# Optimization experiments

Measured on AMD Instinct MI355X. Metric: run time of the kernel, lower is better.

The kernel has to match this reference:

```python
import jax, jax.numpy as jnp
import numpy as np


def expm2(M):
    """Closed-form exponential of a batch of 2x2 matrices M[..., 2, 2].

    exp(M) = e^m * (f*I + g*(M - m*I)) with m = tr(M)/2,
    delta = m^2 - det(M), and (f, g) = (cosh s, sinh s / s) if delta >= 0
    else (cos s, sin s / s) with s = sqrt(|delta|). Identical math to
    torch.matrix_exp for 2x2 inputs.
    """
    a, b, c, d = M[..., 0, 0], M[..., 0, 1], M[..., 1, 0], M[..., 1, 1]
    m = 0.5 * (a + d)
    delta = m * m - (a * d - b * c)
    s = jnp.sqrt(jnp.abs(delta))
    s_safe = jnp.maximum(s, 1e-12)
    pos = delta >= 0
    f = jnp.where(pos, jnp.cosh(s), jnp.cos(s))
    g = jnp.where(pos, jnp.sinh(s_safe), jnp.sin(s_safe)) / s_safe
    em = jnp.exp(m)
    I = jnp.eye(2, dtype=M.dtype)
    N = M - m[..., None, None] * I
    return em[..., None, None] * (f[..., None, None] * I + g[..., None, None] * N)


def setup_inputs() -> dict:
    key = jax.random.key(0)
    k_x0, = jax.random.split(key, 1)
    T, B = 8192, 4096
    t = jnp.arange(T, dtype=jnp.float32) * 0.01  # monotone time grid
    x0 = jax.random.normal(k_x0, (2, B), dtype=jnp.float32)
    return {
        "t": t,
        "x0": x0,
        "omega_sq": jnp.float32(1.2),
        "gamma_0": jnp.float32(0.35),
        "gamma_amp": jnp.float32(0.15),
        "omega_d": jnp.float32(1.1),
    }


def reference(t, x0, omega_sq, gamma_0, gamma_amp, omega_d):
    # Magnus-0 midpoint rule: x_i = exp(dt_i * A(t_mid_i)) @ x_{i-1}
    dt = t[1:] - t[:-1]                      # [T-1]
    tm = t[:-1] + 0.5 * dt                   # midpoint times
    gamma = gamma_0 * (1.0 + gamma_amp * jnp.sin(omega_d * tm))
    zeros = jnp.zeros_like(dt)
    # M_i = dt_i * A(tm_i) = [[0, dt], [-omega_sq*dt, -gamma*dt]]
    M = jnp.stack(
        [jnp.stack([zeros, dt], axis=-1),
         jnp.stack([-omega_sq * dt, -gamma * dt], axis=-1)],
        axis=-2,
    )  # [T-1, 2, 2]
    E = expm2(M)                             # [T-1, 2, 2] step propagators

    def step(x, Ei):
        xn = Ei @ x                          # [2, B]
        return xn, xn

    _, traj = jax.lax.scan(step, x0, E)      # [T-1, 2, B]
    return jnp.concatenate([x0[None], traj], axis=0)  # [T, 2, B]
```

## Files before the change

kernel.cpp:

```cpp
#include <hip/hip_runtime.h>
#include <math.h>


#define CS    64
#define TPB   256
#define MAXCH 256

typedef float fvec2 __attribute__((ext_vector_type(2)));

__global__ __launch_bounds__(64) void chunk_E(
        const float* __restrict__ t,
        const float* __restrict__ p_w2,
        const float* __restrict__ p_g0,
        const float* __restrict__ p_gamp,
        const float* __restrict__ p_od,
        float4* __restrict__ E,
        double* __restrict__ M,
        int nsteps) {
    const int c = blockIdx.x;
    const int j = c * CS + threadIdx.x;
    double e00 = 1.0, e01 = 0.0, e10 = 0.0, e11 = 1.0;
    if (j < nsteps) {
        double w2 = (double)p_w2[0], g0 = (double)p_g0[0];
        double gamp = (double)p_gamp[0], od = (double)p_od[0];
        double t0 = (double)t[j], t1 = (double)t[j + 1];
        double dt = t1 - t0;
        double tm = t0 + 0.5 * dt;
        double gamma = g0 * (1.0 + gamp * sin(od * tm));
        double m = -0.5 * gamma * dt;
        double delta = m * m - w2 * dt * dt;
        double s = sqrt(fabs(delta));
        double ss = fmax(s, 1e-12);
        double f, g;
        if (delta >= 0.0) {
            f = cosh(s); g = sinh(ss) / ss;
        } else {
            double sn, cz;
            sincos(ss, &sn, &cz);
            f = cz; g = sn / ss;
        }
        double em = exp(m);
        e00 = em * (f - g * m);
        e01 = em * (g * dt);
        e10 = em * (-g * w2 * dt);
        e11 = em * (f + g * m);
        E[j] = make_float4((float)e00, (float)e01, (float)e10, (float)e11);
    }
    #pragma unroll
    for (int k = 0; k < 6; ++k) {
        const int hi = (threadIdx.x >> k) & 1;
        double p00 = __shfl_xor(e00, 1 << k, 64);
        double p01 = __shfl_xor(e01, 1 << k, 64);
        double p10 = __shfl_xor(e10, 1 << k, 64);
        double p11 = __shfl_xor(e11, 1 << k, 64);
        double a00 = hi ? e00 : p00, a01 = hi ? e01 : p01;
        double a10 = hi ? e10 : p10, a11 = hi ? e11 : p11;
        double b00 = hi ? p00 : e00, b01 = hi ? p01 : e01;
        double b10 = hi ? p10 : e10, b11 = hi ? p11 : e11;
        e00 = a00 * b00 + a01 * b10;
        e01 = a00 * b01 + a01 * b11;
        e10 = a10 * b00 + a11 * b10;
        e11 = a10 * b01 + a11 * b11;
    }
    if (threadIdx.x == 0) {
        M[4 * c + 0] = e00; M[4 * c + 1] = e01;
        M[4 * c + 2] = e10; M[4 * c + 3] = e11;
    }
}

__global__ __launch_bounds__(TPB) void propagate(
        const float4* __restrict__ E,
        const double* __restrict__ M,
        const float* __restrict__ x0,
        float* __restrict__ out,
        int nsteps, int B, int bgroups) {
    __shared__ float4 Es[CS];
    __shared__ double Ml[MAXCH][4];
    __shared__ double qsh[4];
    const int c   = blockIdx.x / bgroups;
    const int bg  = blockIdx.x % bgroups;
    const int tid = threadIdx.x;
    const int j0  = c * CS;
    const int n   = min(CS, nsteps - j0);

    if (tid < n) Es[tid] = E[j0 + tid];
    for (int i = tid; i < 4 * c; i += TPB)
        Ml[i >> 2][i & 3] = M[i];
    __syncthreads();

    if (tid == 0) {
        double q00 = 1, q01 = 0, q10 = 0, q11 = 1;
        for (int cc = 0; cc < c; ++cc) {
            double a00 = Ml[cc][0], a01 = Ml[cc][1];
            double a10 = Ml[cc][2], a11 = Ml[cc][3];
            double n00 = a00 * q00 + a01 * q10;
            double n01 = a00 * q01 + a01 * q11;
            double n10 = a10 * q00 + a11 * q10;
            double n11 = a10 * q01 + a11 * q11;
            q00 = n00; q01 = n01; q10 = n10; q11 = n11;
        }
        qsh[0] = q00; qsh[1] = q01; qsh[2] = q10; qsh[3] = q11;
    }
    __syncthreads();
    const float q00 = (float)qsh[0], q01 = (float)qsh[1];
    const float q10 = (float)qsh[2], q11 = (float)qsh[3];

    const int b = 2 * (bg * TPB + tid);
    if (b >= B) return;

    const float2 xr0 = *(const float2*)(x0 + b);
    const float2 xr1 = *(const float2*)(x0 + B + b);
    float a0 = q00 * xr0.x + q01 * xr1.x;
    float c0 = q10 * xr0.x + q11 * xr1.x;
    float a1 = q00 * xr0.y + q01 * xr1.y;
    float c1 = q10 * xr0.y + q11 * xr1.y;

    if (c == 0) {
        *(float2*)(out + b) = xr0;
        *(float2*)(out + B + b) = xr1;
    }

    float* o = out + (size_t)(j0 + 1) * 2 * (size_t)B + b;
    #pragma unroll 4
    for (int jj = 0; jj < n; ++jj) {
        float4 e = Es[jj];
        float na0 = e.x * a0 + e.y * c0;
        float nc0 = e.z * a0 + e.w * c0;
        float na1 = e.x * a1 + e.y * c1;
        float nc1 = e.z * a1 + e.w * c1;
        a0 = na0; c0 = nc0; a1 = na1; c1 = nc1;
        fvec2 r0; r0.x = a0; r0.y = a1;
        fvec2 r1; r1.x = c0; r1.y = c1;
        __builtin_nontemporal_store(r0, (fvec2*)o);
        __builtin_nontemporal_store(r1, (fvec2*)(o + B));
        o += 2 * B;
    }
}

extern "C" void kernel_launch(void* const* d_in, const int* in_sizes, int n_in,
                              void* d_out, int out_size, void* d_ws, size_t ws_size,
                              hipStream_t stream) {
    const float* t    = (const float*)d_in[0];
    const float* x0   = (const float*)d_in[1];
    const float* w2   = (const float*)d_in[2];
    const float* g0   = (const float*)d_in[3];
    const float* gamp = (const float*)d_in[4];
    const float* od   = (const float*)d_in[5];
    float* out = (float*)d_out;

    const int T = in_sizes[0];
    const int B = in_sizes[1] / 2;
    const int nsteps = T - 1;
    const int nch = (nsteps + CS - 1) / CS;
    const int bgroups = (B + 2 * TPB - 1) / (2 * TPB);

    float4* E = (float4*)d_ws;
    double* M = (double*)((char*)d_ws + (((size_t)nsteps * 16 + 255) & ~(size_t)255));

    chunk_E<<<nch, 64, 0, stream>>>(t, w2, g0, gamp, od, E, M, nsteps);
    propagate<<<nch * bgroups, TPB, 0, stream>>>(E, M, x0, out, nsteps, B, bgroups);
}
```

Before: 274.6 us.

## Parallel prefix-scan chunk propagators and widen per-thread columns to four

Replaces the serial single-thread product of prior chunk matrices with a block-wide Hillis-Steele scan over all chunk propagators in shared memory. It also makes each thread own four batch columns, using 128-bit nontemporal stores and halving the block count. The goal is to remove the O(nch) serial prologue in late-chunk blocks and to raise store width and per-thread ILP. In exchange every block now scans all chunks, paying about log2(nch) barriers, and there are fewer threads per output row.

```diff
diff --git a/kernel.cpp b/kernel.cpp
--- a/kernel.cpp
+++ b/kernel.cpp
@@ -4,9 +4,10 @@
 
 #define CS    64
 #define TPB   256
+#define CPT   4
 #define MAXCH 256
 
-typedef float fvec2 __attribute__((ext_vector_type(2)));
+typedef float fvec4 __attribute__((ext_vector_type(4)));
 
 __global__ __launch_bounds__(64) void chunk_E(
         const float* __restrict__ t,
@@ -73,10 +74,9 @@
         const double* __restrict__ M,
         const float* __restrict__ x0,
         float* __restrict__ out,
-        int nsteps, int B, int bgroups) {
+        int nsteps, int B, int bgroups, int nch) {
     __shared__ float4 Es[CS];
-    __shared__ double Ml[MAXCH][4];
-    __shared__ double qsh[4];
+    __shared__ double Pl[MAXCH][5];
     const int c   = blockIdx.x / bgroups;
     const int bg  = blockIdx.x % bgroups;
     const int tid = threadIdx.x;
@@ -84,55 +84,70 @@
     const int n   = min(CS, nsteps - j0);
 
     if (tid < n) Es[tid] = E[j0 + tid];
-    for (int i = tid; i < 4 * c; i += TPB)
-        Ml[i >> 2][i & 3] = M[i];
+    for (int i = tid; i < 4 * nch; i += TPB)
+        Pl[i >> 2][i & 3] = M[i];
     __syncthreads();
 
-    if (tid == 0) {
-        double q00 = 1, q01 = 0, q10 = 0, q11 = 1;
-        for (int cc = 0; cc < c; ++cc) {
-            double a00 = Ml[cc][0], a01 = Ml[cc][1];
-            double a10 = Ml[cc][2], a11 = Ml[cc][3];
-            double n00 = a00 * q00 + a01 * q10;
-            double n01 = a00 * q01 + a01 * q11;
-            double n10 = a10 * q00 + a11 * q10;
-            double n11 = a10 * q01 + a11 * q11;
-            q00 = n00; q01 = n01; q10 = n10; q11 = n11;
+    double p00 = 0, p01 = 0, p10 = 0, p11 = 0;
+    if (tid < nch) {
+        p00 = Pl[tid][0]; p01 = Pl[tid][1]; p10 = Pl[tid][2]; p11 = Pl[tid][3];
+    }
+    for (int d = 1; d < nch; d <<= 1) {
+        double b00 = 0, b01 = 0, b10 = 0, b11 = 0;
+        const bool act = (tid >= d) && (tid < nch);
+        if (act) {
+            b00 = Pl[tid - d][0]; b01 = Pl[tid - d][1];
+            b10 = Pl[tid - d][2]; b11 = Pl[tid - d][3];
         }
-        qsh[0] = q00; qsh[1] = q01; qsh[2] = q10; qsh[3] = q11;
+        __syncthreads();
+        if (act) {
+            double n00 = p00 * b00 + p01 * b10;
+            double n01 = p00 * b01 + p01 * b11;
+            double n10 = p10 * b00 + p11 * b10;
+            double n11 = p10 * b01 + p11 * b11;
+            p00 = n00; p01 = n01; p10 = n10; p11 = n11;
+            Pl[tid][0] = p00; Pl[tid][1] = p01; Pl[tid][2] = p10; Pl[tid][3] = p11;
+        }
+        __syncthreads();
     }
-    __syncthreads();
-    const float q00 = (float)qsh[0], q01 = (float)qsh[1];
-    const float q10 = (float)qsh[2], q11 = (float)qsh[3];
+    float q00, q01, q10, q11;
+    if (c == 0) { q00 = 1.f; q01 = 0.f; q10 = 0.f; q11 = 1.f; }
+    else {
+        q00 = (float)Pl[c - 1][0]; q01 = (float)Pl[c - 1][1];
+        q10 = (float)Pl[c - 1][2]; q11 = (float)Pl[c - 1][3];
+    }
 
-    const int b = 2 * (bg * TPB + tid);
+    const int b = CPT * (bg * TPB + tid);
     if (b >= B) return;
 
-    const float2 xr0 = *(const float2*)(x0 + b);
-    const float2 xr1 = *(const float2*)(x0 + B + b);
-    float a0 = q00 * xr0.x + q01 * xr1.x;
-    float c0 = q10 * xr0.x + q11 * xr1.x;
-    float a1 = q00 * xr0.y + q01 * xr1.y;
-    float c1 = q10 * xr0.y + q11 * xr1.y;
+    const float4 xr0 = *(const float4*)(x0 + b);
+    const float4 xr1 = *(const float4*)(x0 + B + b);
+    float a0 = q00 * xr0.x + q01 * xr1.x, c0 = q10 * xr0.x + q11 * xr1.x;
+    float a1 = q00 * xr0.y + q01 * xr1.y, c1 = q10 * xr0.y + q11 * xr1.y;
+    float a2 = q00 * xr0.z + q01 * xr1.z, c2 = q10 * xr0.z + q11 * xr1.z;
+    float a3 = q00 * xr0.w + q01 * xr1.w, c3 = q10 * xr0.w + q11 * xr1.w;
 
     if (c == 0) {
-        *(float2*)(out + b) = xr0;
-        *(float2*)(out + B + b) = xr1;
+        fvec4 z0 = { xr0.x, xr0.y, xr0.z, xr0.w };
+        fvec4 z1 = { xr1.x, xr1.y, xr1.z, xr1.w };
+        __builtin_nontemporal_store(z0, (fvec4*)(out + b));
+        __builtin_nontemporal_store(z1, (fvec4*)(out + B + b));
     }
 
     float* o = out + (size_t)(j0 + 1) * 2 * (size_t)B + b;
     #pragma unroll 4
     for (int jj = 0; jj < n; ++jj) {
         float4 e = Es[jj];
-        float na0 = e.x * a0 + e.y * c0;
-        float nc0 = e.z * a0 + e.w * c0;
-        float na1 = e.x * a1 + e.y * c1;
-        float nc1 = e.z * a1 + e.w * c1;
+        float na0 = e.x * a0 + e.y * c0, nc0 = e.z * a0 + e.w * c0;
+        float na1 = e.x * a1 + e.y * c1, nc1 = e.z * a1 + e.w * c1;
+        float na2 = e.x * a2 + e.y * c2, nc2 = e.z * a2 + e.w * c2;
+        float na3 = e.x * a3 + e.y * c3, nc3 = e.z * a3 + e.w * c3;
         a0 = na0; c0 = nc0; a1 = na1; c1 = nc1;
-        fvec2 r0; r0.x = a0; r0.y = a1;
-        fvec2 r1; r1.x = c0; r1.y = c1;
-        __builtin_nontemporal_store(r0, (fvec2*)o);
-        __builtin_nontemporal_store(r1, (fvec2*)(o + B));
+        a2 = na2; c2 = nc2; a3 = na3; c3 = nc3;
+        fvec4 r0 = { a0, a1, a2, a3 };
+        fvec4 r1 = { c0, c1, c2, c3 };
+        __builtin_nontemporal_store(r0, (fvec4*)o);
+        __builtin_nontemporal_store(r1, (fvec4*)(o + B));
         o += 2 * B;
     }
 }
@@ -152,11 +167,11 @@
     const int B = in_sizes[1] / 2;
     const int nsteps = T - 1;
     const int nch = (nsteps + CS - 1) / CS;
-    const int bgroups = (B + 2 * TPB - 1) / (2 * TPB);
+    const int bgroups = (B + CPT * TPB - 1) / (CPT * TPB);
 
     float4* E = (float4*)d_ws;
     double* M = (double*)((char*)d_ws + (((size_t)nsteps * 16 + 255) & ~(size_t)255));
 
     chunk_E<<<nch, 64, 0, stream>>>(t, w2, g0, gamp, od, E, M, nsteps);
-    propagate<<<nch * bgroups, TPB, 0, stream>>>(E, M, x0, out, nsteps, B, bgroups);
+    propagate<<<nch * bgroups, TPB, 0, stream>>>(E, M, x0, out, nsteps, B, bgroups, nch);
 }
```

After: 304.6 us. +10.9%, slower.
